# Optimization experiments

Measured on AMD Instinct MI355X. Metric: run time of the kernel, lower is better.

Reference implementation:

```python
import jax, jax.numpy as jnp
import numpy as np

B, LS, LW, LV, M, D, H = 256, 1024, 1024, 1024, 16, 5120, 2048

def setup_inputs() -> dict:
    key = jax.random.key(0)
    ks = jax.random.split(key, 8)
    return {
        'phi_batch': jax.random.normal(ks[0], (B, LS), jnp.float32),
        'w_M_real': jax.random.normal(ks[1], (B, LW, M), jnp.float32),
        'w_M_imag': jax.random.normal(ks[2], (B, LW, M), jnp.float32),
        'v_M': jax.random.normal(ks[3], (LV, M), jnp.float32),
        'W1e': jax.random.normal(ks[4], (D, H), jnp.float32) * 0.02,
        'b1e': jnp.zeros((H,), jnp.float32),
        'W2e': jax.random.normal(ks[5], (H, LS), jnp.float32) * 0.02,
        'b2e': jnp.zeros((LS,), jnp.float32),
        'W1r': jax.random.normal(ks[6], (D, H), jnp.float32) * 0.02,
        'b1r': jnp.zeros((H,), jnp.float32),
        'W2r': jax.random.normal(ks[7], (H, 1), jnp.float32) * 0.02,
        'b2r': jnp.zeros((1,), jnp.float32),
    }

def reference(phi_batch, w_M_real, w_M_imag, v_M, W1e, b1e, W2e, b2e, W1r, b1r, W2r, b2r):
    b, ls = phi_batch.shape
    m = v_M.shape[1]
    # s = (1/sqrt(Ls)) * exp(1j*phi); use real/imag parts directly
    mag = 1.0 / jnp.sqrt(jnp.asarray(ls, jnp.float32))
    s_feat = jnp.concatenate([mag * jnp.cos(phi_batch), mag * jnp.sin(phi_batch)], axis=-1)  # [B, 2Ls]
    # Batched concat across (batch, M): replaces the nested Python loops
    X = jnp.concatenate([
        jnp.broadcast_to(s_feat[:, None, :], (b, m, s_feat.shape[-1])),
        jnp.swapaxes(w_M_real, 1, 2),                       # [B, M, Lw]
        jnp.swapaxes(w_M_imag, 1, 2),                       # [B, M, Lw]
        jnp.broadcast_to(v_M.T[None, :, :], (b, m, v_M.shape[0])),
    ], axis=-1)                                             # [B, M, D]
    eta_M = jax.nn.relu(X @ W1e + b1e) @ W2e + b2e          # [B, M, Ls]
    rho_M = (jax.nn.relu(X @ W1r + b1r) @ W2r + b2r)[..., 0]  # [B, M]
    eta = jnp.einsum('bm,bml->bl', rho_M, eta_M)            # sum_m rho_m * eta_m
    phi_optimal = phi_batch - eta
    return phi_optimal, jnp.swapaxes(eta_M, 1, 2)           # [B, Ls], [B, Ls, M]
```

## Files before the change

### kernel.cpp

```cpp
#include <hip/hip_runtime.h>
#include <hip/hip_bf16.h>
#include <stdint.h>

#define B_    256
#define LS_   1024
#define LW_   1024
#define LV_   1024
#define M_    16
#define D_    5120
#define H_    2048
#define ROWS  4096
#define N1    4096
#define KW    2048

typedef __hip_bfloat16 bf16;
typedef __bf16 bf16x8 __attribute__((ext_vector_type(8)));
typedef __bf16 bf16x4 __attribute__((ext_vector_type(4)));
typedef float f32x4 __attribute__((ext_vector_type(4)));

#define SB0() __builtin_amdgcn_sched_barrier(0)
#define LGKM(n) asm volatile("s_waitcnt lgkmcnt(" #n ")" ::: "memory")
#define VMC(n)  asm volatile("s_waitcnt vmcnt(" #n ")" ::: "memory")
#define BARv()  __builtin_amdgcn_s_barrier()

__device__ __forceinline__ void gld_lds16(const void* g, void* l) {
  auto gp = (const __attribute__((address_space(1))) uint32_t*)(uintptr_t)g;
  auto lp = (__attribute__((address_space(3))) uint32_t*)(uint32_t)(uintptr_t)l;
  __builtin_amdgcn_global_load_lds(gp, lp, 16, 0, 0);
}

__device__ __forceinline__ void transpose64_body(char* sm, const float* __restrict__ in,
                                                 bf16* __restrict__ out,
                                                 int C, int R, int r0, int c0, int t) {
  float (*tile)[65] = (float (*)[65])sm;
  const int tx = t & 15, ty = t >> 4;
#pragma unroll
  for (int i = 0; i < 4; ++i) {
    const float4 v = *(const float4*)&in[(size_t)(r0 + ty + i * 16) * C + c0 + tx * 4];
    tile[ty + i * 16][tx * 4 + 0] = v.x;
    tile[ty + i * 16][tx * 4 + 1] = v.y;
    tile[ty + i * 16][tx * 4 + 2] = v.z;
    tile[ty + i * 16][tx * 4 + 3] = v.w;
  }
  __syncthreads();
#pragma unroll
  for (int i = 0; i < 4; ++i) {
    const int n = c0 + ty + i * 16;
    bf16x4 o;
#pragma unroll
    for (int j = 0; j < 4; ++j) o[j] = (__bf16)tile[tx * 4 + j][ty + i * 16];
    *(bf16x4*)&out[(size_t)n * R + r0 + tx * 4] = o;
  }
}

__global__ void __launch_bounds__(256)
prep_kernel(const float* __restrict__ phi,
            const float* __restrict__ wMr, const float* __restrict__ wMi,
            const float* __restrict__ vM,
            const float* __restrict__ W1e, const float* __restrict__ W1r,
            const float* __restrict__ W2e,
            bf16* __restrict__ sfeat, bf16* __restrict__ Awr,
            bf16* __restrict__ W1sT, bf16* __restrict__ W1wT,
            bf16* __restrict__ W2t, float* __restrict__ hVT) {
  __shared__ __align__(16) char sm[32768];
  const int bid = blockIdx.x;
  const int t = threadIdx.x;

  if (bid < 256) {
    float (*vs)[16] = (float (*)[16])sm;
    float (*ws)[16] = (float (*)[16])(sm + 16384);
    const float* Wb = (bid < 128) ? W1e : W1r;
    const int nbase = (bid & 127) * 16;
    const int nout = ((bid < 128) ? 0 : 2048) + nbase;
    const int m = t & 15, nl = t >> 4;
    float acc = 0.f;
    for (int l0 = 0; l0 < 1024; l0 += 256) {
      __syncthreads();
#pragma unroll
      for (int i = 0; i < 16; ++i) {
        int e = i * 256 + t, l = e >> 4, n = e & 15;
        vs[l][n] = vM[(size_t)(l0 + l) * 16 + n];
        ws[l][n] = Wb[(size_t)(4096 + l0 + l) * 2048 + nbase + n];
      }
      __syncthreads();
#pragma unroll 8
      for (int ll = 0; ll < 256; ++ll)
        acc += vs[ll][m] * ws[ll][nl];
    }
    hVT[(size_t)(nout + nl) * 16 + m] = acc;
  } else if (bid < 4352) {
    const int idx = bid - 256;
    const int z = idx >> 10, rem = idx & 1023;
    const float* src = (z == 0 || z == 2) ? W1e : W1r;
    src += (z < 2) ? 0 : (size_t)2048 * 2048;
    bf16* dst = (z < 2) ? W1sT : W1wT;
    dst += (z == 0 || z == 2) ? 0 : (size_t)2048 * 2048;
    transpose64_body(sm, src, dst, 2048, 2048, (rem >> 5) * 64, (rem & 31) * 64, t);
  } else if (bid < 4864) {
    const int idx = bid - 4352;
    transpose64_body(sm, W2e, W2t, LS_, H_, (idx >> 4) * 64, (idx & 15) * 64, t);
  } else if (bid < 8960) {
    const int idx = bid - 4864;
    const int b = idx >> 4, l0 = (idx & 15) * 64;
    float (*tr)[17] = (float (*)[17])sm;
    float (*ti)[17] = (float (*)[17])(sm + 4352 * 4);
    const float* wrb = wMr + (size_t)b * (LW_ * M_) + (size_t)l0 * 16;
    const float* wib = wMi + (size_t)b * (LW_ * M_) + (size_t)l0 * 16;
#pragma unroll
    for (int i = 0; i < 4; ++i) {
      int e = i * 256 + t, l = e >> 4, m = e & 15;
      tr[l][m] = wrb[e];
      ti[l][m] = wib[e];
    }
    __syncthreads();
    int m = t >> 4, t4 = t & 15;
    bf16* outR = Awr + (size_t)(b * 16 + m) * KW + l0;
#pragma unroll
    for (int j = 0; j < 4; ++j) outR[t4 * 4 + j]        = __float2bfloat16(tr[t4 * 4 + j][m]);
#pragma unroll
    for (int j = 0; j < 4; ++j) outR[1024 + t4 * 4 + j] = __float2bfloat16(ti[t4 * 4 + j][m]);
  } else {
    const int i = (bid - 8960) * 256 + t;
    const int b = i >> 10, l = i & 1023;
    float p = phi[i];
    float s, c;
    sincosf(p, &s, &c);
    sfeat[b * 2048 + l]        = __float2bfloat16(0.03125f * c);
    sfeat[b * 2048 + 1024 + l] = __float2bfloat16(0.03125f * s);
  }
}

__global__ void __launch_bounds__(512, 2)
gemm1_256_kernel(const bf16* __restrict__ A, const bf16* __restrict__ Bt,
                 const float* __restrict__ hSp, const float* __restrict__ hVT,
                 const float* __restrict__ bias0, const float* __restrict__ bias1,
                 const float* __restrict__ w2r,
                 bf16* __restrict__ outH, float* __restrict__ rhoP) {
  extern __shared__ __align__(16) char smem[];
  constexpr int NKT = KW / 64;
  constexpr int NI  = NKT / 2;

  const int tid  = threadIdx.x;
  const int lane = tid & 63;
  const int wave = tid >> 6;
  const int wr = wave >> 2, wc = wave & 3;
  const int fr = lane & 15, fq = lane >> 4;
  const int row0 = blockIdx.y * 256, col0 = blockIdx.x * 256;

  float* tblHS = (float*)(smem + 131072);

  {
    const int e0 = tid * 8;
    const int bgl = e0 >> 8, cl = e0 & 255;
    const int bg = (row0 >> 4) + bgl;
    const int ce = col0 + cl;
    const float* p = hSp + (size_t)bg * N1 + ce;
    f32x4 s0 = *(const f32x4*)p;
    f32x4 s1 = *(const f32x4*)(p + 4);
    s0 = s0 + *(const f32x4*)(p + (size_t)B_ * N1);
    s1 = s1 + *(const f32x4*)(p + (size_t)B_ * N1 + 4);
    s0 = s0 + *(const f32x4*)(p + (size_t)2 * B_ * N1);
    s1 = s1 + *(const f32x4*)(p + (size_t)2 * B_ * N1 + 4);
    s0 = s0 + *(const f32x4*)(p + (size_t)3 * B_ * N1);
    s1 = s1 + *(const f32x4*)(p + (size_t)3 * B_ * N1 + 4);
    const float* bp = (ce < H_) ? &bias0[ce] : &bias1[ce - H_];
    s0 = s0 + *(const f32x4*)bp;
    s1 = s1 + *(const f32x4*)(bp + 4);
    *(f32x4*)&tblHS[e0]     = s0;
    *(f32x4*)&tblHS[e0 + 4] = s1;
  }
  VMC(0);
  SB0();

  const int xr  = fr & 7;
  const int sK0 = ((fq ^ xr) << 4);
  const int sK1 = (((4 + fq) ^ xr) << 4);
  const int aRowB = (wr * 128 + fr) << 7;
  const int bRowB = 32768 + ((wc * 64 + fr) << 7);

  const char* gA = (const char*)A  + (size_t)row0 * (KW * 2);
  const char* gB = (const char*)Bt + (size_t)col0 * (KW * 2);
  char* buf0 = smem;
  char* buf1 = smem + 65536;

  const int srow  = tid >> 3;
  const int slotU = (tid & 7) ^ (srow & 7);

  auto stageHalf = [&](const char* g, char* ldsOp, int half, int kt) {
#pragma unroll
    for (int r = 0; r < 2; ++r) {
      const int row = half * 128 + r * 64 + srow;
      gld_lds16(g + (size_t)row * (KW * 2) + (size_t)kt * 128 + slotU * 16,
                ldsOp + half * 16384 + r * 8192 + tid * 16);
    }
  };

  f32x4 acc[8][4] = {};

  auto readA4 = [&](const char* buf, int mg, int sk, bf16x8 (&a)[4]) {
    const char* p = buf + aRowB + mg * 8192 + sk;
#pragma unroll
    for (int i = 0; i < 4; ++i) a[i] = *(const bf16x8*)(p + i * 2048);
  };
  auto readB4 = [&](const char* buf, int sk, bf16x8 (&b)[4]) {
    const char* p = buf + bRowB + sk;
#pragma unroll
    for (int n = 0; n < 4; ++n) b[n] = *(const bf16x8*)(p + n * 2048);
  };
  auto mma16 = [&](int mg, bf16x8 (&a)[4], bf16x8 (&b)[4]) {
    __builtin_amdgcn_s_setprio(1);
#pragma unroll
    for (int i = 0; i < 4; ++i)
#pragma unroll
      for (int n = 0; n < 4; ++n)
        acc[mg * 4 + i][n] =
            __builtin_amdgcn_mfma_f32_16x16x32_bf16(a[i], b[n], acc[mg * 4 + i][n], 0, 0, 0);
    __builtin_amdgcn_s_setprio(0);
  };

  stageHalf(gB, buf0 + 32768, 0, 0);
  stageHalf(gB, buf0 + 32768, 1, 0);
  stageHalf(gA, buf0, 0, 0);
  stageHalf(gA, buf0, 1, 0);
  stageHalf(gB, buf1 + 32768, 0, 1);
  VMC(2);
  BARv();

  for (int t = 0; t < NI; ++t) {
    const int k1 = 2 * t + 1;
    const bool pf = (t + 1 < NI);
    bf16x8 aX[4], aY[4], b0[4], b1[4];

    readA4(buf0, 0, sK0, aX); readB4(buf0, sK0, b0);
    stageHalf(gB, buf1 + 32768, 1, k1);
    BARv(); LGKM(0); SB0();
    mma16(0, aX, b0);
    SB0(); BARv();

    readA4(buf0, 1, sK0, aY);
    stageHalf(gA, buf1, 0, k1);
    BARv(); LGKM(0); SB0();
    mma16(1, aY, b0);
    SB0(); BARv();

    readA4(buf0, 0, sK1, aX); readB4(buf0, sK1, b1);
    stageHalf(gA, buf1, 1, k1);
    BARv(); LGKM(0); SB0();
    mma16(0, aX, b1);
    SB0(); BARv();

    readA4(buf0, 1, sK1, aY);
    if (pf) { stageHalf(gB, buf0 + 32768, 0, 2 * t + 2); VMC(2); }
    else    { VMC(0); }
    BARv(); LGKM(0); SB0();
    mma16(1, aY, b1);
    SB0(); BARv();

    readA4(buf1, 0, sK0, aX); readB4(buf1, sK0, b0);
    if (pf) stageHalf(gB, buf0 + 32768, 1, 2 * t + 2);
    BARv(); LGKM(0); SB0();
    mma16(0, aX, b0);
    SB0(); BARv();

    readA4(buf1, 1, sK0, aY);
    if (pf) stageHalf(gA, buf0, 0, 2 * t + 2);
    BARv(); LGKM(0); SB0();
    mma16(1, aY, b0);
    SB0(); BARv();

    readA4(buf1, 0, sK1, aX); readB4(buf1, sK1, b1);
    if (pf) stageHalf(gA, buf0, 1, 2 * t + 2);
    BARv(); LGKM(0); SB0();
    mma16(0, aX, b1);
    SB0(); BARv();

    readA4(buf1, 1, sK1, aY);
    if (pf) { stageHalf(gB, buf1 + 32768, 0, 2 * t + 3); VMC(2); }
    else    { VMC(0); }
    BARv(); LGKM(0); SB0();
    mma16(1, aY, b1);
    SB0(); BARv();
  }

  if (col0 < H_) {
#pragma unroll
    for (int n = 0; n < 4; ++n) {
      const int c = col0 + wc * 64 + n * 16 + fr;
      const int clo = wc * 64 + n * 16 + fr;
      const f32x4 hv = *(const f32x4*)&hVT[(size_t)c * 16 + fq * 4];
#pragma unroll
      for (int m = 0; m < 8; ++m) {
        const int rbase = row0 + wr * 128 + m * 16;
        const float hs = tblHS[(wr * 8 + m) * 256 + clo];
#pragma unroll
        for (int j = 0; j < 4; ++j) {
          const int r = rbase + fq * 4 + j;
          float v = acc[m][n][j] + hs + hv[j];
          outH[(size_t)r * N1 + c] = __float2bfloat16(v > 0.f ? v : 0.f);
        }
      }
    }
  } else {
    const int cb = (col0 >> 8) - 8;
    float* rhoT = (float*)smem;
    f32x4 hv4[4];
    float w2[4];
#pragma unroll
    for (int n = 0; n < 4; ++n) {
      const int c = col0 + wc * 64 + n * 16 + fr;
      hv4[n] = *(const f32x4*)&hVT[(size_t)c * 16 + fq * 4];
      w2[n] = w2r[c - H_];
    }
#pragma unroll
    for (int m = 0; m < 8; ++m) {
      f32x4 rsv = {0.f, 0.f, 0.f, 0.f};
#pragma unroll
      for (int n = 0; n < 4; ++n) {
        const int clo = wc * 64 + n * 16 + fr;
        const float hs = tblHS[(wr * 8 + m) * 256 + clo];
#pragma unroll
        for (int j = 0; j < 4; ++j) {
          float v = acc[m][n][j] + hs + hv4[n][j];
          v = v > 0.f ? v : 0.f;
          rsv[j] += v * w2[n];
        }
      }
#pragma unroll
      for (int j = 0; j < 4; ++j) {
        rsv[j] += __shfl_xor(rsv[j], 1);
        rsv[j] += __shfl_xor(rsv[j], 2);
        rsv[j] += __shfl_xor(rsv[j], 4);
        rsv[j] += __shfl_xor(rsv[j], 8);
      }
      if (fr == 0)
        *(f32x4*)&rhoT[((wr * 4 + wc) << 7) + m * 16 + fq * 4] = rsv;
    }
    __syncthreads();
    if (tid < 256) {
      const int wrr = tid >> 7, lr = tid & 127;
      const float* rt = &rhoT[(wrr * 4) << 7];
      const float s = rt[lr] + rt[128 + lr] + rt[256 + lr] + rt[384 + lr];
      rhoP[(size_t)(row0 + wrr * 128 + lr) * 8 + cb] = s;
    }
  }
}

template <int EPI, int NT>
__global__ void __launch_bounds__(256, 2)
gemm128_pipe_kernel(const bf16* __restrict__ A, int lda,
                    const bf16* __restrict__ Bt, int ldb,
                    const float* __restrict__ bias0,
                    const float* __restrict__ rhoP, const float* __restrict__ b2r,
                    const float* __restrict__ phi,
                    float* __restrict__ outS, float* __restrict__ out0) {
  extern __shared__ __align__(16) char smem[];

  if (EPI == 1) {
    const int z = blockIdx.z;
    A    += (size_t)z * 512;
    Bt   += (size_t)z * 512;
    outS += (size_t)z * ((size_t)B_ * N1);
  }

  const int tid  = threadIdx.x;
  const int lane = tid & 63;
  const int wave = tid >> 6;
  const int wr = wave >> 1, wc = wave & 1;
  const int fr = lane & 15, fq = lane >> 4;
  const int row0 = blockIdx.y * 128, col0 = blockIdx.x * 128;

  if (EPI == 0) {
    if (tid < 128) {
      const float* pp = &rhoP[(size_t)(row0 + tid) * 8];
      const f32x4 p0 = *(const f32x4*)pp;
      const f32x4 p1 = *(const f32x4*)(pp + 4);
      const float s = p0[0] + p0[1] + p0[2] + p0[3] +
                      p1[0] + p1[1] + p1[2] + p1[3] + b2r[0];
      ((float*)(smem + 65536))[tid] = s;
    }
    LGKM(0);
    SB0();
  }

  const int slotF = (((fr & 1) << 2) | fq) ^ ((fr >> 1) & 7);
  const int aOff = (wr << 12) + ((fr >> 1) << 7) + (slotF << 4);
  const int bOff = 8192 + (wc << 12) + ((fr >> 1) << 7) + (slotF << 4);

  const int lgl = tid >> 3;
  const int su  = (tid & 7) ^ (lgl & 7);
  const int rp0 = lgl * 2 + (su >> 2);
  const int rp1 = (32 + lgl) * 2 + (su >> 2);
  const int kb  = (su & 3) << 4;
  const char* pA0 = (const char*)A  + (size_t)(row0 + rp0) * ((size_t)lda * 2) + kb;
  const char* pA1 = (const char*)A  + (size_t)(row0 + rp1) * ((size_t)lda * 2) + kb;
  const char* pB0 = (const char*)Bt + (size_t)(col0 + rp0) * ((size_t)ldb * 2) + kb;
  const char* pB1 = (const char*)Bt + (size_t)(col0 + rp1) * ((size_t)ldb * 2) + kb;

  auto stageTile = [&](int T) {
    char* dst = smem + (size_t)(T & 3) * 16384;
    const size_t ko = (size_t)T * 64;
    gld_lds16(pA0 + ko, dst + 0     + tid * 16);
    gld_lds16(pA1 + ko, dst + 4096  + tid * 16);
    gld_lds16(pB0 + ko, dst + 8192  + tid * 16);
    gld_lds16(pB1 + ko, dst + 12288 + tid * 16);
  };

  f32x4 acc[4][4] = {};
  bf16x8 aA[4], aB[4], bA[4], bB[4];

  stageTile(0); stageTile(1); stageTile(2);
  VMC(4);
  __builtin_amdgcn_s_barrier();
  {
    const char* aP0 = smem + aOff;
    const char* bP0 = smem + bOff;
#pragma unroll
    for (int m = 0; m < 4; ++m) aA[m] = *(const bf16x8*)(aP0 + m * 1024);
#pragma unroll
    for (int n = 0; n < 4; ++n) bA[n] = *(const bf16x8*)(bP0 + n * 1024);
  }
  SB0();

  auto doIter = [&](int T, bf16x8 (&aCur)[4], bf16x8 (&bCur)[4],
                    bf16x8 (&aNxt)[4], bf16x8 (&bNxt)[4]) {
    const char* aPn = smem + (size_t)((T + 1) & 3) * 16384 + aOff;
    const char* bPn = smem + (size_t)((T + 1) & 3) * 16384 + bOff;
    const bool rb = (T + 1 < NT);
    const bool pf = (T + 3 < NT);

    if (pf) stageTile(T + 3);
    LGKM(0);
    SB0();
    if (rb) {
#pragma unroll
      for (int m = 0; m < 4; ++m) aNxt[m] = *(const bf16x8*)(aPn + m * 1024);
#pragma unroll
      for (int n = 0; n < 4; ++n) bNxt[n] = *(const bf16x8*)(bPn + n * 1024);
    }
    SB0();
    __builtin_amdgcn_s_setprio(1);
#pragma unroll
    for (int m = 0; m < 4; ++m)
#pragma unroll
      for (int n = 0; n < 4; ++n)
        acc[m][n] = __builtin_amdgcn_mfma_f32_16x16x32_bf16(aCur[m], bCur[n], acc[m][n], 0, 0, 0);
    __builtin_amdgcn_s_setprio(0);
    SB0();
    if (pf) { VMC(4); }
    else    { VMC(0); }
    __builtin_amdgcn_s_barrier();
  };

  for (int t = 0; t < NT; t += 2) {
    doIter(t,     aA, bA, aB, bB);
    doIter(t + 1, aB, bB, aA, bA);
  }

  if (EPI == 0) {
    const float* rhoL = (const float*)(smem + 65536);
#pragma unroll
    for (int m = 0; m < 4; ++m) {
      const int bg = (row0 >> 4) + wr * 4 + m;
      const f32x4 rv = *(const f32x4*)&rhoL[wr * 64 + m * 16 + fq * 4];
#pragma unroll
      for (int n = 0; n < 4; ++n) {
        const int c = col0 + wc * 64 + n * 16 + fr;
        const float bias = bias0[c];
        float part = 0.f;
#pragma unroll
        for (int j = 0; j < 4; ++j) {
          float v = acc[m][n][j] + bias;
          outS[(size_t)bg * (LS_ * M_) + (size_t)c * M_ + (fq * 4 + j)] = v;
          part += rv[j] * v;
        }
        part += __shfl_xor(part, 16);
        part += __shfl_xor(part, 32);
        if (fq == 0)
          out0[(size_t)bg * LS_ + c] = phi[(size_t)bg * LS_ + c] - part;
      }
    }
  } else {
#pragma unroll
    for (int m = 0; m < 4; ++m) {
#pragma unroll
      for (int n = 0; n < 4; ++n) {
        const int c = col0 + wc * 64 + n * 16 + fr;
#pragma unroll
        for (int j = 0; j < 4; ++j) {
          const int r = row0 + wr * 64 + m * 16 + fq * 4 + j;
          outS[(size_t)r * N1 + c] = acc[m][n][j];
        }
      }
    }
  }
}

extern "C" void kernel_launch(void* const* d_in, const int* in_sizes, int n_in,
                              void* d_out, int out_size, void* d_ws, size_t ws_size,
                              hipStream_t stream) {
  const float* phi = (const float*)d_in[0];
  const float* wMr = (const float*)d_in[1];
  const float* wMi = (const float*)d_in[2];
  const float* vM  = (const float*)d_in[3];
  const float* W1e = (const float*)d_in[4];
  const float* b1e = (const float*)d_in[5];
  const float* W2e = (const float*)d_in[6];
  const float* b2e = (const float*)d_in[7];
  const float* W1r = (const float*)d_in[8];
  const float* b1r = (const float*)d_in[9];
  const float* W2r = (const float*)d_in[10];
  const float* b2r = (const float*)d_in[11];

  float* out0 = (float*)d_out;
  float* out1 = out0 + (size_t)B_ * LS_;

  bf16* Awr   = (bf16*)d_ws;
  bf16* W1sT  = Awr  + (size_t)ROWS * KW;
  bf16* W1wT  = W1sT + (size_t)N1 * KW;
  bf16* h     = W1wT + (size_t)N1 * KW;
  bf16* W2t   = h + (size_t)ROWS * N1;
  bf16* sfeat = W2t + (size_t)LS_ * H_;
  float* hSp  = (float*)(sfeat + (size_t)B_ * 2048);
  float* hVT  = hSp + (size_t)4 * B_ * N1;
  float* rhoP = hVT + (size_t)N1 * 16;

  (void)hipFuncSetAttribute(reinterpret_cast<const void*>(gemm1_256_kernel),
                            hipFuncAttributeMaxDynamicSharedMemorySize, 147456);
  (void)hipFuncSetAttribute(reinterpret_cast<const void*>(gemm128_pipe_kernel<0, 64>),
                            hipFuncAttributeMaxDynamicSharedMemorySize, 66048);
  (void)hipFuncSetAttribute(reinterpret_cast<const void*>(gemm128_pipe_kernel<1, 16>),
                            hipFuncAttributeMaxDynamicSharedMemorySize, 65536);

  prep_kernel<<<9984, 256, 0, stream>>>(phi, wMr, wMi, vM, W1e, W1r, W2e,
                                        sfeat, Awr, W1sT, W1wT, W2t, hVT);

  gemm128_pipe_kernel<1, 16><<<dim3(N1 / 128, B_ / 128, 4), 256, 65536, stream>>>(
      sfeat, 2048, W1sT, KW, nullptr, nullptr, nullptr, nullptr, hSp, nullptr);

  gemm1_256_kernel<<<dim3(N1 / 256, ROWS / 256), 512, 147456, stream>>>(
      Awr, W1wT, hSp, hVT, b1e, b1r, W2r, h, rhoP);

  gemm128_pipe_kernel<0, 64><<<dim3(LS_ / 128, ROWS / 128), 256, 66048, stream>>>(
      h, N1, W2t, H_, b2e, rhoP, b2r, phi, out1, out0);
}
```

Baseline: 139.0 us.

## Split K across two wave groups in second GEMM with LDS reduction

```diff
diff --git a/kernel.cpp b/kernel.cpp
--- a/kernel.cpp
+++ b/kernel.cpp
@@ -345,22 +345,152 @@
   }
 }
 
-template <int EPI, int NT>
+__global__ void __launch_bounds__(512, 2)
+gemm2_8w_kernel(const bf16* __restrict__ A, int lda,
+                const bf16* __restrict__ Bt, int ldb,
+                const float* __restrict__ bias0,
+                const float* __restrict__ rhoP, const float* __restrict__ b2r,
+                const float* __restrict__ phi,
+                float* __restrict__ outS, float* __restrict__ out0) {
+  extern __shared__ __align__(16) char smem[];
+  constexpr int NT = 64;
+
+  const int tid  = threadIdx.x;
+  const int lane = tid & 63;
+  const int wave = tid >> 6;
+  const int kh = wave >> 2;
+  const int w2 = wave & 3;
+  const int wr = w2 >> 1, wc = w2 & 1;
+  const int fr = lane & 15, fq = lane >> 4;
+  const int row0 = blockIdx.y * 128, col0 = blockIdx.x * 128;
+
+  float* rhoL = (float*)(smem + 98304);
+
+  if (tid < 128) {
+    const float* pp = &rhoP[(size_t)(row0 + tid) * 8];
+    const f32x4 p0 = *(const f32x4*)pp;
+    const f32x4 p1 = *(const f32x4*)(pp + 4);
+    rhoL[tid] = p0[0] + p0[1] + p0[2] + p0[3] +
+                p1[0] + p1[1] + p1[2] + p1[3] + b2r[0];
+  }
+  VMC(0); LGKM(0);
+  SB0();
+
+  const int slotF = (((fr & 1) << 2) | fq) ^ ((fr >> 1) & 7);
+  const int aOff = (wr << 12) + ((fr >> 1) << 7) + (slotF << 4);
+  const int bOff = 8192 + (wc << 12) + ((fr >> 1) << 7) + (slotF << 4);
+
+  const int sline = tid >> 3;
+  const int sls   = tid & 7;
+  const int ssu   = sls ^ (sline & 7);
+  const int srowi = (sline >> 3) * 16 + (sline & 7) * 2 + (ssu >> 2);
+  const int skb   = (ssu & 3) << 4;
+  const char* pAg = (const char*)A  + (size_t)(row0 + srowi) * ((size_t)lda * 2) + skb;
+  const char* pBg = (const char*)Bt + (size_t)(col0 + srowi) * ((size_t)ldb * 2) + skb;
+
+  auto stageTile = [&](int T, int slot) {
+    char* dst = smem + (size_t)slot * 16384;
+    const size_t ko = (size_t)T * 64;
+    gld_lds16(pAg + ko, dst + tid * 16);
+    gld_lds16(pBg + ko, dst + 8192 + tid * 16);
+  };
+
+  f32x4 acc[4][4] = {};
+
+  stageTile(0, 0); stageTile(1, 1); stageTile(2, 2); stageTile(3, 3);
+  VMC(4);
+  BARv();
+
+  int s0 = 0;
+  for (int i = 0; i < 32; ++i) {
+    const char* buf = smem + (size_t)(s0 + kh) * 16384;
+    const char* aP = buf + aOff;
+    const char* bP = buf + bOff;
+    bf16x8 a[4], b[4];
+#pragma unroll
+    for (int m = 0; m < 4; ++m) a[m] = *(const bf16x8*)(aP + m * 1024);
+#pragma unroll
+    for (int n = 0; n < 4; ++n) b[n] = *(const bf16x8*)(bP + n * 1024);
+    SB0();
+    if (i < 30) {
+      const int sA = (s0 >= 2) ? s0 - 2 : 4;
+      stageTile(2 * i + 4, sA);
+      stageTile(2 * i + 5, (sA + 1 == 6) ? 0 : sA + 1);
+    }
+    SB0();
+    LGKM(0);
+    SB0();
+    __builtin_amdgcn_s_setprio(1);
+#pragma unroll
+    for (int m = 0; m < 4; ++m)
+#pragma unroll
+      for (int n = 0; n < 4; ++n)
+        acc[m][n] = __builtin_amdgcn_mfma_f32_16x16x32_bf16(a[m], b[n], acc[m][n], 0, 0, 0);
+    __builtin_amdgcn_s_setprio(0);
+    SB0();
+    if (i < 30) { VMC(4); }
+    else        { VMC(0); }
+    BARv();
+    s0 = (s0 == 4) ? 0 : s0 + 2;
+  }
+
+  if (kh == 1) {
+    char* base = smem + (((w2 << 6) + lane) << 8);
+#pragma unroll
+    for (int m = 0; m < 4; ++m)
+#pragma unroll
+      for (int n = 0; n < 4; ++n) {
+        const int idx = (m * 4 + n) ^ (lane & 15);
+        *(f32x4*)(base + idx * 16) = acc[m][n];
+      }
+  }
+  LGKM(0);
+  BARv();
+  if (kh == 0) {
+    const char* base = smem + (((w2 << 6) + lane) << 8);
+#pragma unroll
+    for (int m = 0; m < 4; ++m)
+#pragma unroll
+      for (int n = 0; n < 4; ++n) {
+        const int idx = (m * 4 + n) ^ (lane & 15);
+        acc[m][n] = acc[m][n] + *(const f32x4*)(base + idx * 16);
+      }
+
+#pragma unroll
+    for (int m = 0; m < 4; ++m) {
+      const int bg = (row0 >> 4) + wr * 4 + m;
+      const f32x4 rv = *(const f32x4*)&rhoL[wr * 64 + m * 16 + fq * 4];
+#pragma unroll
+      for (int n = 0; n < 4; ++n) {
+        const int c = col0 + wc * 64 + n * 16 + fr;
+        const float bias = bias0[c];
+        float part = 0.f;
+#pragma unroll
+        for (int j = 0; j < 4; ++j) {
+          float v = acc[m][n][j] + bias;
+          outS[(size_t)bg * (LS_ * M_) + (size_t)c * M_ + (fq * 4 + j)] = v;
+          part += rv[j] * v;
+        }
+        part += __shfl_xor(part, 16);
+        part += __shfl_xor(part, 32);
+        if (fq == 0)
+          out0[(size_t)bg * LS_ + c] = phi[(size_t)bg * LS_ + c] - part;
+      }
+    }
+  }
+}
+
+template <int NT>
 __global__ void __launch_bounds__(256, 2)
-gemm128_pipe_kernel(const bf16* __restrict__ A, int lda,
-                    const bf16* __restrict__ Bt, int ldb,
-                    const float* __restrict__ bias0,
-                    const float* __restrict__ rhoP, const float* __restrict__ b2r,
-                    const float* __restrict__ phi,
-                    float* __restrict__ outS, float* __restrict__ out0) {
+gemmS_pipe_kernel(const bf16* __restrict__ A, int lda,
+                  const bf16* __restrict__ Bt, int ldb,
+                  float* __restrict__ outS) {
   extern __shared__ __align__(16) char smem[];
 
-  if (EPI == 1) {
-    const int z = blockIdx.z;
-    A    += (size_t)z * 512;
-    Bt   += (size_t)z * 512;
-    outS += (size_t)z * ((size_t)B_ * N1);
-  }
+  const int z = blockIdx.z;
+  A    += (size_t)z * 512;
+  Bt   += (size_t)z * 512;
+  outS += (size_t)z * ((size_t)B_ * N1);
 
   const int tid  = threadIdx.x;
   const int lane = tid & 63;
@@ -368,19 +498,6 @@
   const int wr = wave >> 1, wc = wave & 1;
   const int fr = lane & 15, fq = lane >> 4;
   const int row0 = blockIdx.y * 128, col0 = blockIdx.x * 128;
-
-  if (EPI == 0) {
-    if (tid < 128) {
-      const float* pp = &rhoP[(size_t)(row0 + tid) * 8];
-      const f32x4 p0 = *(const f32x4*)pp;
-      const f32x4 p1 = *(const f32x4*)(pp + 4);
-      const float s = p0[0] + p0[1] + p0[2] + p0[3] +
-                      p1[0] + p1[1] + p1[2] + p1[3] + b2r[0];
-      ((float*)(smem + 65536))[tid] = s;
-    }
-    LGKM(0);
-    SB0();
-  }
 
   const int slotF = (((fr & 1) << 2) | fq) ^ ((fr >> 1) & 7);
   const int aOff = (wr << 12) + ((fr >> 1) << 7) + (slotF << 4);
@@ -456,40 +573,15 @@
     doIter(t + 1, aB, bB, aA, bA);
   }
 
-  if (EPI == 0) {
-    const float* rhoL = (const float*)(smem + 65536);
-#pragma unroll
-    for (int m = 0; m < 4; ++m) {
-      const int bg = (row0 >> 4) + wr * 4 + m;
-      const f32x4 rv = *(const f32x4*)&rhoL[wr * 64 + m * 16 + fq * 4];
-#pragma unroll
-      for (int n = 0; n < 4; ++n) {
-        const int c = col0 + wc * 64 + n * 16 + fr;
-        const float bias = bias0[c];
-        float part = 0.f;
-#pragma unroll
-        for (int j = 0; j < 4; ++j) {
-          float v = acc[m][n][j] + bias;
-          outS[(size_t)bg * (LS_ * M_) + (size_t)c * M_ + (fq * 4 + j)] = v;
-          part += rv[j] * v;
-        }
-        part += __shfl_xor(part, 16);
-        part += __shfl_xor(part, 32);
-        if (fq == 0)
-          out0[(size_t)bg * LS_ + c] = phi[(size_t)bg * LS_ + c] - part;
-      }
-    }
-  } else {
-#pragma unroll
-    for (int m = 0; m < 4; ++m) {
-#pragma unroll
-      for (int n = 0; n < 4; ++n) {
-        const int c = col0 + wc * 64 + n * 16 + fr;
-#pragma unroll
-        for (int j = 0; j < 4; ++j) {
-          const int r = row0 + wr * 64 + m * 16 + fq * 4 + j;
-          outS[(size_t)r * N1 + c] = acc[m][n][j];
-        }
+#pragma unroll
+  for (int m = 0; m < 4; ++m) {
+#pragma unroll
+    for (int n = 0; n < 4; ++n) {
+      const int c = col0 + wc * 64 + n * 16 + fr;
+#pragma unroll
+      for (int j = 0; j < 4; ++j) {
+        const int r = row0 + wr * 64 + m * 16 + fq * 4 + j;
+        outS[(size_t)r * N1 + c] = acc[m][n][j];
       }
     }
   }
@@ -526,20 +618,20 @@
 
   (void)hipFuncSetAttribute(reinterpret_cast<const void*>(gemm1_256_kernel),
                             hipFuncAttributeMaxDynamicSharedMemorySize, 147456);
-  (void)hipFuncSetAttribute(reinterpret_cast<const void*>(gemm128_pipe_kernel<0, 64>),
-                            hipFuncAttributeMaxDynamicSharedMemorySize, 66048);
-  (void)hipFuncSetAttribute(reinterpret_cast<const void*>(gemm128_pipe_kernel<1, 16>),
+  (void)hipFuncSetAttribute(reinterpret_cast<const void*>(gemm2_8w_kernel),
+                            hipFuncAttributeMaxDynamicSharedMemorySize, 98816);
+  (void)hipFuncSetAttribute(reinterpret_cast<const void*>(gemmS_pipe_kernel<16>),
                             hipFuncAttributeMaxDynamicSharedMemorySize, 65536);
 
   prep_kernel<<<9984, 256, 0, stream>>>(phi, wMr, wMi, vM, W1e, W1r, W2e,
                                         sfeat, Awr, W1sT, W1wT, W2t, hVT);
 
-  gemm128_pipe_kernel<1, 16><<<dim3(N1 / 128, B_ / 128, 4), 256, 65536, stream>>>(
-      sfeat, 2048, W1sT, KW, nullptr, nullptr, nullptr, nullptr, hSp, nullptr);
+  gemmS_pipe_kernel<16><<<dim3(N1 / 128, B_ / 128, 4), 256, 65536, stream>>>(
+      sfeat, 2048, W1sT, KW, hSp);
 
   gemm1_256_kernel<<<dim3(N1 / 256, ROWS / 256), 512, 147456, stream>>>(
       Awr, W1wT, hSp, hVT, b1e, b1r, W2r, h, rhoP);
 
-  gemm128_pipe_kernel<0, 64><<<dim3(LS_ / 128, ROWS / 128), 256, 66048, stream>>>(
+  gemm2_8w_kernel<<<dim3(LS_ / 128, ROWS / 128), 512, 98816, stream>>>(
       h, N1, W2t, H_, b2e, rhoP, b2r, phi, out1, out0);
 }
```

Result: faster. 133.1 us (-4.2%).
